# Kernel tuning notes

Hardware: AMD Instinct MI355X
Metric: run time of the kernel (lower is better)

The kernel has to match this reference:

```python
import jax, jax.numpy as jnp
import numpy as np

N = 50000      # nodes
E = 800000     # edges (before self-loops)
F_IN = 128     # input features
H = 4          # heads
C = 32         # hidden_dim per head
HC = H * C     # 128, concat width
G = 64         # graphs in batch
OUT = 10       # classes
NEG_SLOPE = 0.2  # PyG GATConv default negative_slope


def setup_inputs() -> dict:
    key = jax.random.key(0)
    ks = jax.random.split(key, 16)
    x = jax.random.normal(ks[0], (N, F_IN), dtype=jnp.float32)
    edge_index = jax.random.randint(ks[1], (2, E), 0, N, dtype=jnp.int32)
    batch = jnp.sort(jax.random.randint(ks[2], (N,), 0, G, dtype=jnp.int32))
    s = 0.05
    Ws = [
        jax.random.normal(ks[3], (F_IN, HC), jnp.float32) * s,
        jax.random.normal(ks[4], (HC, HC), jnp.float32) * s,
        jax.random.normal(ks[5], (HC, HC), jnp.float32) * s,
    ]
    a_srcs = [jax.random.normal(ks[6 + i], (H, C), jnp.float32) * s for i in range(3)]
    a_dsts = [jax.random.normal(ks[9 + i], (H, C), jnp.float32) * s for i in range(3)]
    biases = [jnp.zeros((HC,), jnp.float32) for _ in range(3)]
    Wh = jax.random.normal(ks[12], (HC, OUT), jnp.float32) * s
    bh = jnp.zeros((OUT,), jnp.float32)
    return {"x": x, "Ws": Ws, "a_srcs": a_srcs, "a_dsts": a_dsts,
            "biases": biases, "Wh": Wh, "bh": bh,
            "edge_index": edge_index, "batch": batch}


def gat_layer(x, W, a_src, a_dst, b, src, dst, n):
    # x: [N, F]; W: [F, H*C]; a_src/a_dst: [H, C]
    h = (x @ W).reshape(n, H, C)                     # [N, H, C]
    alpha_s = jnp.sum(h * a_src, axis=-1)            # [N, H]
    alpha_d = jnp.sum(h * a_dst, axis=-1)            # [N, H]
    e = jax.nn.leaky_relu(alpha_s[src] + alpha_d[dst], NEG_SLOPE)  # [E', H]
    # segment softmax over incoming edges (grouped by dst)
    emax = jax.ops.segment_max(e, dst, num_segments=n)             # [N, H]
    ex = jnp.exp(e - emax[dst])
    denom = jax.ops.segment_sum(ex, dst, num_segments=n)
    alpha = ex / denom[dst]                                        # [E', H]
    msg = h[src] * alpha[:, :, None]                               # [E', H, C]
    out = jax.ops.segment_sum(msg, dst, num_segments=n)            # [N, H, C]
    return out.reshape(n, HC) + b


def reference(x, Ws, a_srcs, a_dsts, biases, Wh, bh, edge_index, batch):
    n = x.shape[0]
    # PyG GATConv adds self-loops by default
    loops = jnp.arange(n, dtype=edge_index.dtype)
    src = jnp.concatenate([edge_index[0], loops])
    dst = jnp.concatenate([edge_index[1], loops])
    for i in range(3):
        x = jax.nn.relu(gat_layer(x, Ws[i], a_srcs[i], a_dsts[i], biases[i], src, dst, n))
        # dropout is identity in eval mode
    pooled = jax.ops.segment_sum(x, batch, num_segments=G)  # global_add_pool -> [G, HC]
    logits = pooled @ Wh + bh                                # [G, OUT]
    return logits
```

## Files before the change

### kernel.cpp

```cpp
#include <hip/hip_runtime.h>
#include <hip/hip_bf16.h>

#define HC 128
#define NHEAD 4
#define NEG 0.2f
#define CHUNK 4096

typedef unsigned int uint32;
typedef __attribute__((ext_vector_type(8))) short short8v;
typedef __attribute__((ext_vector_type(4))) float f32x4;

__device__ __forceinline__ float leaky(float v) { return v > 0.f ? v : NEG * v; }
__device__ __forceinline__ int clampi(int v, int lo, int hi) { return v < lo ? lo : (v > hi ? hi : v); }

__device__ __forceinline__ uint32 pack_bf16(float lo, float hi) {
  uint32 a = __float_as_uint(lo);
  uint32 b = __float_as_uint(hi);
  a = (a + 0x7FFFu + ((a >> 16) & 1u)) >> 16;
  b = (b + 0x7FFFu + ((b >> 16) & 1u)) & 0xFFFF0000u;
  return a | b;
}
__device__ __forceinline__ unsigned short bf16_1(float v) {
  uint32 a = __float_as_uint(v);
  return (unsigned short)((a + 0x7FFFu + ((a >> 16) & 1u)) >> 16);
}
__device__ __forceinline__ float2 unpack_bf16(uint32 u) {
  return make_float2(__uint_as_float(u << 16), __uint_as_float(u & 0xFFFF0000u));
}
__device__ __forceinline__ short8v as_s8(uint4 u) {
  union { uint4 a; short8v b; } c; c.a = u; return c.b;
}

#define WT_STRIDE 18432

__global__ __launch_bounds__(256) void zero_kernel(int* __restrict__ p, int n) {
  int i = blockIdx.x * 256 + threadIdx.x;
  int stride = gridDim.x * 256;
  for (; i < n; i += stride) p[i] = 0;
}

__global__ __launch_bounds__(256) void bincnt_lds(const int* __restrict__ dst, int* __restrict__ bcnt, int E, int n) {
  __shared__ int h[256];
  int t = threadIdx.x;
  h[t] = 0;
  __syncthreads();
  int e0 = blockIdx.x * CHUNK;
  int e1 = e0 + CHUNK < E ? e0 + CHUNK : E;
  for (int i = e0 + t; i < e1; i += 256) {
    int d = clampi(dst[i], 0, n - 1);
    atomicAdd(&h[d >> 8], 1);
  }
  __syncthreads();
  if (h[t] > 0) atomicAdd(&bcnt[t], h[t]);
}

__global__ __launch_bounds__(256) void bscan_kernel(const int* __restrict__ bcnt, int* __restrict__ bbase,
                                                    int* __restrict__ bcur, int NBKT) {
  __shared__ int part[256];
  int t = threadIdx.x;
  int c = (t < NBKT) ? bcnt[t] : 0;
  part[t] = c;
  __syncthreads();
  for (int off = 1; off < 256; off <<= 1) {
    int v = (t >= off) ? part[t - off] : 0;
    __syncthreads();
    part[t] += v;
    __syncthreads();
  }
  int excl = part[t] - c;
  if (t < NBKT) {
    bbase[t] = excl;
    bcur[t] = excl;
  }
}

__global__ __launch_bounds__(256) void binscatter_staged(const int* __restrict__ src, const int* __restrict__ dst,
                                                         int* __restrict__ bcur, int2* __restrict__ ebuf, int E, int n) {
  __shared__ int lcnt[256];
  __shared__ int lbase[256];
  int t = threadIdx.x;
  lcnt[t] = 0;
  __syncthreads();
  int e0 = blockIdx.x * CHUNK;
  int e1 = e0 + CHUNK < E ? e0 + CHUNK : E;
  for (int i = e0 + t; i < e1; i += 256) {
    int d = clampi(dst[i], 0, n - 1);
    atomicAdd(&lcnt[d >> 8], 1);
  }
  __syncthreads();
  int myc = lcnt[t];
  lbase[t] = (myc > 0) ? atomicAdd(&bcur[t], myc) : 0;
  __syncthreads();
  lcnt[t] = 0;
  __syncthreads();
  for (int i = e0 + t; i < e1; i += 256) {
    int d = clampi(dst[i], 0, n - 1);
    int s = clampi(src[i], 0, n - 1);
    int b = d >> 8;
    int pos = atomicAdd(&lcnt[b], 1);
    int p = lbase[b] + pos;
    if (p >= 0 && p < E) ebuf[p] = make_int2(s, d);
  }
}

__global__ __launch_bounds__(256) void bucket_finalize(const int2* __restrict__ ebuf, const int* __restrict__ bbase,
                                                       int* __restrict__ row_start, int* __restrict__ csr,
                                                       int NBKT, int E, int n) {
  __shared__ int cnt[256];
  __shared__ int part[256];
  __shared__ int cur[256];
  int b = blockIdx.x;
  int t = threadIdx.x;
  int start = bbase[b];
  int end = (b == NBKT - 1) ? E : bbase[b + 1];
  int d0 = b << 8;
  int ndst = n - d0; if (ndst > 256) ndst = 256;
  cnt[t] = 0;
  __syncthreads();
  for (int i = start + t; i < end; i += 256) {
    int d = ebuf[i].y - d0;
    if (d >= 0 && d < 256) atomicAdd(&cnt[d], 1);
  }
  __syncthreads();
  int c = cnt[t];
  part[t] = c;
  __syncthreads();
  for (int off = 1; off < 256; off <<= 1) {
    int v = (t >= off) ? part[t - off] : 0;
    __syncthreads();
    part[t] += v;
    __syncthreads();
  }
  int excl = part[t] - c;
  if (t < ndst) row_start[d0 + t] = start + excl;
  if (b == NBKT - 1 && t == 0) row_start[n] = E;
  cur[t] = start + excl;
  __syncthreads();
  for (int i = start + t; i < end; i += 256) {
    int2 pr = ebuf[i];
    int d = pr.y - d0;
    if (d >= 0 && d < 256) {
      int p = atomicAdd(&cur[d], 1);
      if (p >= 0 && p < E) csr[p] = pr.x;
    }
  }
}

__global__ __launch_bounds__(256) void hist_kernel(const int* __restrict__ dst, int* __restrict__ cnt, int E, int n) {
  int e = blockIdx.x * 256 + threadIdx.x;
  if (e < E) atomicAdd(&cnt[clampi(dst[e], 0, n - 1)], 1);
}
__global__ __launch_bounds__(256) void scan_pass1(const int* __restrict__ cnt, int* __restrict__ blocksum, int n) {
  __shared__ int red[256];
  int t = threadIdx.x;
  int i = blockIdx.x * 256 + t;
  red[t] = i < n ? cnt[i] : 0;
  __syncthreads();
  for (int off = 128; off >= 1; off >>= 1) {
    if (t < off) red[t] += red[t + off];
    __syncthreads();
  }
  if (t == 0) blocksum[blockIdx.x] = red[0];
}
__global__ __launch_bounds__(256) void scan_pass2(const int* __restrict__ blocksum, int* __restrict__ blockpre,
                                                  int* __restrict__ row_start, int NB, int n) {
  __shared__ int part[256];
  int t = threadIdx.x;
  int chunk = (NB + 255) >> 8;
  int lo = t * chunk; if (lo > NB) lo = NB;
  int hi = lo + chunk; if (hi > NB) hi = NB;
  int s = 0;
  for (int i = lo; i < hi; ++i) s += blocksum[i];
  part[t] = s;
  __syncthreads();
  for (int off = 1; off < 256; off <<= 1) {
    int v = (t >= off) ? part[t - off] : 0;
    __syncthreads();
    part[t] += v;
    __syncthreads();
  }
  int run = part[t] - s;
  for (int i = lo; i < hi; ++i) {
    blockpre[i] = run;
    run += blocksum[i];
  }
  if (t == 255) row_start[n] = part[255];
}
__global__ __launch_bounds__(256) void scan_pass3(const int* __restrict__ cnt, const int* __restrict__ blockpre,
                                                  int* __restrict__ row_start, int* __restrict__ cursor, int n) {
  __shared__ int part[256];
  int t = threadIdx.x;
  int i = blockIdx.x * 256 + t;
  int c = i < n ? cnt[i] : 0;
  part[t] = c;
  __syncthreads();
  for (int off = 1; off < 256; off <<= 1) {
    int v = (t >= off) ? part[t - off] : 0;
    __syncthreads();
    part[t] += v;
    __syncthreads();
  }
  int excl = part[t] - c;
  if (i < n) {
    int b = blockpre[blockIdx.x] + excl;
    row_start[i] = b;
    cursor[i] = b;
  }
}
__global__ __launch_bounds__(256) void scatter_kernel(const int* __restrict__ src, const int* __restrict__ dst,
                                                      int* __restrict__ cursor, int* __restrict__ csr, int E, int n) {
  int e = blockIdx.x * 256 + threadIdx.x;
  if (e < E) {
    int d = clampi(dst[e], 0, n - 1);
    int s = clampi(src[e], 0, n - 1);
    int p = atomicAdd(&cursor[d], 1);
    if (p >= 0 && p < E) csr[p] = s;
  }
}

__global__ __launch_bounds__(256) void prep_kernel(const float* __restrict__ x, const float* __restrict__ W0,
                                                   const float* __restrict__ W1, const float* __restrict__ W2,
                                                   const float* __restrict__ as0, const float* __restrict__ as1,
                                                   const float* __restrict__ as2, const float* __restrict__ ad0,
                                                   const float* __restrict__ ad1, const float* __restrict__ ad2,
                                                   uint32* __restrict__ X16, unsigned short* __restrict__ wt,
                                                   int* __restrict__ bcnt, float* __restrict__ pooled,
                                                   long long n64, int NC, int Gp) {
  long long id = (long long)blockIdx.x * 256 + threadIdx.x;
  if (id < n64) {
    float2 v = *(const float2*)&x[id * 2];
    X16[id] = pack_bf16(v.x, v.y);
    return;
  }
  long long id2l = id - n64;
  if (id2l < 3 * 16384) {
    int id2 = (int)id2l;
    int l = id2 >> 14;
    int r = id2 & 16383;
    int k = r >> 7, nc = r & 127;
    const float* W = l == 0 ? W0 : (l == 1 ? W1 : W2);
    wt[(size_t)l * WT_STRIDE + nc * 128 + k] = bf16_1(W[r]);
    return;
  }
  id2l -= 3 * 16384;
  if (id2l < 3 * 2048) {
    int id2 = (int)id2l;
    int l = id2 >> 11;
    int r = id2 & 2047;
    int col8 = r >> 7, k = r & 127;
    const float* W = l == 0 ? W0 : (l == 1 ? W1 : W2);
    unsigned short outv = 0;
    if (col8 < 8) {
      int h = col8 & 3;
      const float* av = (col8 < 4) ? (l == 0 ? as0 : (l == 1 ? as1 : as2))
                                   : (l == 0 ? ad0 : (l == 1 ? ad1 : ad2));
      float s = 0.f;
      for (int c = 0; c < 32; ++c) s += W[k * 128 + 32 * h + c] * av[32 * h + c];
      outv = bf16_1(s);
    }
    wt[(size_t)l * WT_STRIDE + (128 + col8) * 128 + k] = outv;
    return;
  }
  id2l -= 3 * 2048;
  if (id2l < NC) {
    bcnt[id2l] = 0;
    return;
  }
  id2l -= NC;
  if (id2l < (long long)Gp * 128) pooled[id2l] = 0.f;
}

__global__ __launch_bounds__(256) void gemm_mfma(const uint32* __restrict__ X16, const unsigned short* __restrict__ Wt,
                                                 uint32* __restrict__ H16, float* __restrict__ As,
                                                 float* __restrict__ Ad, int n) {
  int t = threadIdx.x;
  int wave = t >> 6, lane = t & 63;
  int l15 = lane & 15, lg = lane >> 4;
  int row0 = blockIdx.x * 64 + wave * 16;
  int arow = row0 + l15;
  if (arow >= n) arow = n - 1;
  const uint4* xr = (const uint4*)(X16 + (size_t)arow * 64);
  uint4 a[4];
#pragma unroll
  for (int kc = 0; kc < 4; ++kc) a[kc] = xr[kc * 4 + lg];
  f32x4 acc[9];
#pragma unroll
  for (int nb = 0; nb < 9; ++nb) acc[nb] = (f32x4){0.f, 0.f, 0.f, 0.f};
#pragma unroll
  for (int kc = 0; kc < 4; ++kc) {
    uint4 b[9];
#pragma unroll
    for (int nb = 0; nb < 9; ++nb) {
      int ncol = nb * 16 + l15;
      b[nb] = *(const uint4*)(Wt + (size_t)ncol * 128 + kc * 32 + lg * 8);
    }
#pragma unroll
    for (int nb = 0; nb < 9; ++nb)
      acc[nb] = __builtin_amdgcn_mfma_f32_16x16x32_bf16(as_s8(a[kc]), as_s8(b[nb]), acc[nb], 0, 0, 0);
  }
#pragma unroll
  for (int r = 0; r < 4; ++r) {
    int gr = row0 + lg * 4 + r;
    bool ok = gr < n;
#pragma unroll
    for (int nb = 0; nb < 8; ++nb) {
      float mine = acc[nb][r];
      float other = __shfl_xor(mine, 1);
      if (ok && (lane & 1) == 0) H16[(size_t)gr * 64 + nb * 8 + (l15 >> 1)] = pack_bf16(mine, other);
    }
    float av = acc[8][r];
    if (ok && l15 < 4) As[gr * 4 + l15] = av;
    if (ok && l15 >= 4 && l15 < 8) Ad[gr * 4 + (l15 - 4)] = av;
  }
}

template <bool OUTFP32>
__global__ __launch_bounds__(256) void agg_kernel(const uint32* __restrict__ H16, const float* __restrict__ As,
                                                  const float* __restrict__ Ad, const int* __restrict__ row_start,
                                                  const int* __restrict__ csr, const float* __restrict__ bias,
                                                  void* __restrict__ outv, int n) {
  int wid = (blockIdx.x * 256 + threadIdx.x) >> 6;
  int lane = threadIdx.x & 63;
  if (wid >= n) return;
  int base = row_start[wid];
  int deg = row_start[wid + 1] - base;
  if (deg < 0) deg = 0;
  int hsel = lane >> 4;
  float adsel = Ad[wid * 4 + hsel];
  float pself = __expf(leaky(As[wid * 4 + hsel] + adsel));
  float2 hv = unpack_bf16(H16[(size_t)wid * 64 + lane]);
  float den = pself;
  float acc0 = pself * hv.x, acc1 = pself * hv.y;
  for (int chunk = 0; chunk < deg; chunk += 64) {
    int j = chunk + lane;
    int smine = (j < deg) ? clampi(csr[base + j], 0, n - 1) : 0;
    int cnt_ = deg - chunk; if (cnt_ > 64) cnt_ = 64;
    float pm[4];
#pragma unroll
    for (int k = 0; k < 4; ++k) {
      pm[k] = 0.f;
      if (k * 16 < cnt_) {
        int slot = k * 16 + (lane & 15);
        int sk = __shfl(smine, slot);
        float e = As[sk * 4 + hsel];
        pm[k] = (slot < cnt_) ? __expf(leaky(e + adsel)) : 0.f;
      }
    }
#pragma unroll
    for (int k = 0; k < 4; ++k) {
      if (k * 16 >= cnt_) break;
#pragma unroll
      for (int b = 0; b < 2; ++b) {
        int u0 = k * 16 + b * 8;
        if (u0 >= cnt_) break;
        int ss[8];
        float aw[8];
        float2 h2[8];
#pragma unroll
        for (int i = 0; i < 8; ++i) {
          int u = u0 + i;
          int sv = __shfl(smine, u);
          float av = __shfl(pm[k], (lane & 48) + (u & 15));
          ss[i] = (u < cnt_) ? sv : 0;
          aw[i] = (u < cnt_) ? av : 0.f;
        }
#pragma unroll
        for (int i = 0; i < 8; ++i) h2[i] = unpack_bf16(H16[(size_t)((uint32)ss[i] * 64 + lane)]);
#pragma unroll
        for (int i = 0; i < 8; ++i) {
          den += aw[i];
          acc0 += aw[i] * h2[i].x;
          acc1 += aw[i] * h2[i].y;
        }
      }
    }
  }
  float inv = 1.f / den;
  float2 bv = *(const float2*)&bias[2 * lane];
  float r0v = fmaxf(acc0 * inv + bv.x, 0.f);
  float r1v = fmaxf(acc1 * inv + bv.y, 0.f);
  if constexpr (OUTFP32) {
    ((float2*)outv)[(size_t)wid * 64 + lane] = make_float2(r0v, r1v);
  } else {
    ((uint32*)outv)[(size_t)wid * 64 + lane] = pack_bf16(r0v, r1v);
  }
}

__global__ __launch_bounds__(128) void pool_kernel(const float* __restrict__ X, const int* __restrict__ batch,
                                                   float* __restrict__ pooled, int n, int G) {
  int c = threadIdx.x;
  int n0 = blockIdx.x * 64;
  if (n0 >= n) return;
  int end = n0 + 64 < n ? n0 + 64 : n;
  int curg = clampi(batch[n0], 0, G - 1);
  float acc = 0.f;
  for (int i = n0; i < end; ++i) {
    int g = clampi(batch[i], 0, G - 1);
    if (g != curg) {
      atomicAdd(&pooled[curg * 128 + c], acc);
      acc = 0.f;
      curg = g;
    }
    acc += X[(size_t)i * 128 + c];
  }
  atomicAdd(&pooled[curg * 128 + c], acc);
}

__global__ __launch_bounds__(64) void logits_kernel(const float* __restrict__ pooled, const float* __restrict__ Wh,
                                                    const float* __restrict__ bh, float* __restrict__ out) {
  int g = blockIdx.x, lane = threadIdx.x;
  float p0 = pooled[g * 128 + lane];
  float p1 = pooled[g * 128 + lane + 64];
  for (int o = 0; o < 10; ++o) {
    float v = p0 * Wh[lane * 10 + o] + p1 * Wh[(lane + 64) * 10 + o];
#pragma unroll
    for (int off = 32; off >= 1; off >>= 1) v += __shfl_xor(v, off);
    if (lane == 0) out[g * 10 + o] = v + bh[o];
  }
}

extern "C" void kernel_launch(void* const* d_in, const int* in_sizes, int n_in,
                              void* d_out, int out_size, void* d_ws, size_t ws_size,
                              hipStream_t stream) {
  const float *x, *Wl[3], *asr[3], *adr[3], *bias[3], *Wh, *bh;
  const int *edge_index, *batch;
  long long E_ll;
  if (n_in >= 17) {
    x = (const float*)d_in[0];
    for (int l = 0; l < 3; ++l) {
      Wl[l] = (const float*)d_in[1 + l];
      asr[l] = (const float*)d_in[4 + l];
      adr[l] = (const float*)d_in[7 + l];
      bias[l] = (const float*)d_in[10 + l];
    }
    Wh = (const float*)d_in[13];
    bh = (const float*)d_in[14];
    edge_index = (const int*)d_in[15];
    batch = (const int*)d_in[16];
    E_ll = (long long)in_sizes[15] / 2;
  } else if (n_in >= 9) {
    x = (const float*)d_in[0];
    const float* Wc = (const float*)d_in[1];
    const float* ac = (const float*)d_in[2];
    const float* dc = (const float*)d_in[3];
    const float* bc = (const float*)d_in[4];
    for (int l = 0; l < 3; ++l) {
      Wl[l] = Wc + (size_t)l * HC * HC;
      asr[l] = ac + (size_t)l * HC;
      adr[l] = dc + (size_t)l * HC;
      bias[l] = bc + (size_t)l * HC;
    }
    Wh = (const float*)d_in[5];
    bh = (const float*)d_in[6];
    edge_index = (const int*)d_in[7];
    batch = (const int*)d_in[8];
    E_ll = (long long)in_sizes[7] / 2;
  } else {
    zero_kernel<<<(out_size + 255) / 256, 256, 0, stream>>>((int*)d_out, out_size);
    return;
  }
  int N = in_sizes[0] / HC;
  int G = out_size / 10;
  if (N <= 0 || G <= 0 || E_ll <= 0 || E_ll > (1LL << 30)) {
    zero_kernel<<<(out_size + 255) / 256, 256, 0, stream>>>((int*)d_out, out_size);
    return;
  }
  int E = (int)E_ll;
  int NBKT = (N + 255) >> 8;
  int NB = (N + 255) / 256;
  bool staged = (NBKT <= 256);

  char* w = (char*)d_ws;
  size_t off = 0;
  auto take = [&](size_t bytes) -> char* {
    char* p = w + off;
    off = (off + bytes + 511) & ~(size_t)511;
    return p;
  };
  uint32* H16 = (uint32*)take((size_t)N * 64 * 4);
  uint32* X16 = (uint32*)take((size_t)N * 64 * 4);
  float* bufQ = (float*)take((size_t)N * HC * 4);
  uint32* Xa = (uint32*)bufQ;
  float* As = (float*)take((size_t)N * NHEAD * 4);
  float* Ad = (float*)take((size_t)N * NHEAD * 4);
  int* row_start = (int*)take((size_t)(N + 1) * 4);
  int* csr = (int*)take((size_t)E * 4);
  int2* ebuf = (int2*)take((size_t)E * 8);
  int* bcnt = (int*)take(256 * 4);
  int* bbase = (int*)take(256 * 4);
  int* bcur = (int*)take(256 * 4);
  int* cnt = (int*)take((size_t)N * 4);
  int* cursor = (int*)take((size_t)N * 4);
  int* blocksum = (int*)take((size_t)NB * 4);
  int* blockpre = (int*)take((size_t)NB * 4);
  float* pooled = (float*)take((size_t)G * HC * 4);
  unsigned short* wt16 = (unsigned short*)take((size_t)3 * WT_STRIDE * 2);

  if (off > ws_size) {
    zero_kernel<<<(out_size + 255) / 256, 256, 0, stream>>>((int*)d_out, out_size);
    return;
  }

  const int* esrc = edge_index;
  const int* edst = edge_index + E;

  long long n64 = (long long)N * 64;
  long long prep_items = n64 + 3 * 16384 + 3 * 2048 + 256 + (long long)G * 128;
  prep_kernel<<<(int)((prep_items + 255) / 256), 256, 0, stream>>>(
      x, Wl[0], Wl[1], Wl[2], asr[0], asr[1], asr[2], adr[0], adr[1], adr[2], Xa, wt16, bcnt, pooled, n64, 256, G);

  int echunks = (E + CHUNK - 1) / CHUNK;
  if (staged) {
    bincnt_lds<<<echunks, 256, 0, stream>>>(edst, bcnt, E, N);
    bscan_kernel<<<1, 256, 0, stream>>>(bcnt, bbase, bcur, NBKT);
    binscatter_staged<<<echunks, 256, 0, stream>>>(esrc, edst, bcur, ebuf, E, N);
    bucket_finalize<<<NBKT, 256, 0, stream>>>(ebuf, bbase, row_start, csr, NBKT, E, N);
  } else {
    zero_kernel<<<(N + 255) / 256, 256, 0, stream>>>(cnt, N);
    hist_kernel<<<(E + 255) / 256, 256, 0, stream>>>(edst, cnt, E, N);
    scan_pass1<<<NB, 256, 0, stream>>>(cnt, blocksum, N);
    scan_pass2<<<1, 256, 0, stream>>>(blocksum, blockpre, row_start, NB, N);
    scan_pass3<<<NB, 256, 0, stream>>>(cnt, blockpre, row_start, cursor, N);
    scatter_kernel<<<(E + 255) / 256, 256, 0, stream>>>(esrc, edst, cursor, csr, E, N);
  }

  int gemm_grid = (N + 63) / 64;
  int agg_grid = (N + 3) / 4;

  gemm_mfma<<<gemm_grid, 256, 0, stream>>>(Xa, wt16, H16, As, Ad, N);
  agg_kernel<false><<<agg_grid, 256, 0, stream>>>(H16, As, Ad, row_start, csr, bias[0], X16, N);
  gemm_mfma<<<gemm_grid, 256, 0, stream>>>(X16, wt16 + WT_STRIDE, H16, As, Ad, N);
  agg_kernel<false><<<agg_grid, 256, 0, stream>>>(H16, As, Ad, row_start, csr, bias[1], X16, N);
  gemm_mfma<<<gemm_grid, 256, 0, stream>>>(X16, wt16 + 2 * WT_STRIDE, H16, As, Ad, N);
  agg_kernel<true><<<agg_grid, 256, 0, stream>>>(H16, As, Ad, row_start, csr, bias[2], bufQ, N);

  pool_kernel<<<(N + 63) / 64, 128, 0, stream>>>(bufQ, batch, pooled, N, G);
  logits_kernel<<<G, 64, 0, stream>>>(pooled, Wh, bh, (float*)d_out);
}
```

Baseline: 277.9 us.

## Split GEMM column tiles across waves, fuse pooling with logits, trim agg bounds checks

The GEMM kernel now gives each pair of waves one 16-row tile and splits its 9 output column blocks 5/4 between them. This halves rows per block, doubles the grid and lowers per-wave register pressure. Pooling and the head projection are fused: each block reduces its per-graph partial sums through LDS, multiplies by Wh and atomically adds into the output, which prep_kernel pre-initialises with the bias. This removes the pooled buffer and the separate logits launch. The aggregation kernel drops the source-index clamp and per-slot validity selects, relying on zero-padded shuffled weights, which risks out-of-range reads if the CSR holds bad indices.

```diff
diff --git a/kernel.cpp b/kernel.cpp
--- a/kernel.cpp
+++ b/kernel.cpp
@@ -223,9 +223,9 @@
                                                    const float* __restrict__ as0, const float* __restrict__ as1,
                                                    const float* __restrict__ as2, const float* __restrict__ ad0,
                                                    const float* __restrict__ ad1, const float* __restrict__ ad2,
-                                                   uint32* __restrict__ X16, unsigned short* __restrict__ wt,
-                                                   int* __restrict__ bcnt, float* __restrict__ pooled,
-                                                   long long n64, int NC, int Gp) {
+                                                   const float* __restrict__ bh, uint32* __restrict__ X16,
+                                                   unsigned short* __restrict__ wt, int* __restrict__ bcnt,
+                                                   float* __restrict__ outp, long long n64, int NC, int Gp) {
   long long id = (long long)blockIdx.x * 256 + threadIdx.x;
   if (id < n64) {
     float2 v = *(const float2*)&x[id * 2];
@@ -267,7 +267,7 @@
     return;
   }
   id2l -= NC;
-  if (id2l < (long long)Gp * 128) pooled[id2l] = 0.f;
+  if (id2l < (long long)Gp * 10) outp[id2l] = bh[id2l % 10];
 }
 
 __global__ __launch_bounds__(256) void gemm_mfma(const uint32* __restrict__ X16, const unsigned short* __restrict__ Wt,
@@ -276,41 +276,48 @@
   int t = threadIdx.x;
   int wave = t >> 6, lane = t & 63;
   int l15 = lane & 15, lg = lane >> 4;
-  int row0 = blockIdx.x * 64 + wave * 16;
+  int grp = wave >> 1, half = wave & 1;
+  int row0 = blockIdx.x * 32 + grp * 16;
   int arow = row0 + l15;
   if (arow >= n) arow = n - 1;
   const uint4* xr = (const uint4*)(X16 + (size_t)arow * 64);
   uint4 a[4];
 #pragma unroll
   for (int kc = 0; kc < 4; ++kc) a[kc] = xr[kc * 4 + lg];
-  f32x4 acc[9];
-#pragma unroll
-  for (int nb = 0; nb < 9; ++nb) acc[nb] = (f32x4){0.f, 0.f, 0.f, 0.f};
+  const int NT = half ? 4 : 5;
+  f32x4 acc[5];
+#pragma unroll
+  for (int ti = 0; ti < 5; ++ti) acc[ti] = (f32x4){0.f, 0.f, 0.f, 0.f};
 #pragma unroll
   for (int kc = 0; kc < 4; ++kc) {
-    uint4 b[9];
-#pragma unroll
-    for (int nb = 0; nb < 9; ++nb) {
-      int ncol = nb * 16 + l15;
-      b[nb] = *(const uint4*)(Wt + (size_t)ncol * 128 + kc * 32 + lg * 8);
-    }
-#pragma unroll
-    for (int nb = 0; nb < 9; ++nb)
-      acc[nb] = __builtin_amdgcn_mfma_f32_16x16x32_bf16(as_s8(a[kc]), as_s8(b[nb]), acc[nb], 0, 0, 0);
+    uint4 b[5];
+#pragma unroll
+    for (int ti = 0; ti < 5; ++ti) {
+      if (ti < NT) {
+        int basecol = half ? (4 + ti) * 16 : (ti < 4 ? ti * 16 : 128);
+        b[ti] = *(const uint4*)(Wt + (size_t)(basecol + l15) * 128 + kc * 32 + lg * 8);
+      }
+    }
+#pragma unroll
+    for (int ti = 0; ti < 5; ++ti)
+      if (ti < NT) acc[ti] = __builtin_amdgcn_mfma_f32_16x16x32_bf16(as_s8(a[kc]), as_s8(b[ti]), acc[ti], 0, 0, 0);
   }
 #pragma unroll
   for (int r = 0; r < 4; ++r) {
     int gr = row0 + lg * 4 + r;
     bool ok = gr < n;
 #pragma unroll
-    for (int nb = 0; nb < 8; ++nb) {
-      float mine = acc[nb][r];
+    for (int ti = 0; ti < 4; ++ti) {
+      int nb = half * 4 + ti;
+      float mine = acc[ti][r];
       float other = __shfl_xor(mine, 1);
       if (ok && (lane & 1) == 0) H16[(size_t)gr * 64 + nb * 8 + (l15 >> 1)] = pack_bf16(mine, other);
     }
-    float av = acc[8][r];
-    if (ok && l15 < 4) As[gr * 4 + l15] = av;
-    if (ok && l15 >= 4 && l15 < 8) Ad[gr * 4 + (l15 - 4)] = av;
+    if (half == 0) {
+      float av = acc[4][r];
+      if (ok && l15 < 4) As[gr * 4 + l15] = av;
+      if (ok && l15 >= 4 && l15 < 8) Ad[gr * 4 + (l15 - 4)] = av;
+    }
   }
 }
 
@@ -333,7 +340,7 @@
   float acc0 = pself * hv.x, acc1 = pself * hv.y;
   for (int chunk = 0; chunk < deg; chunk += 64) {
     int j = chunk + lane;
-    int smine = (j < deg) ? clampi(csr[base + j], 0, n - 1) : 0;
+    int smine = (j < deg) ? csr[base + j] : 0;
     int cnt_ = deg - chunk; if (cnt_ > 64) cnt_ = 64;
     float pm[4];
 #pragma unroll
@@ -358,11 +365,8 @@
         float2 h2[8];
 #pragma unroll
         for (int i = 0; i < 8; ++i) {
-          int u = u0 + i;
-          int sv = __shfl(smine, u);
-          float av = __shfl(pm[k], (lane & 48) + (u & 15));
-          ss[i] = (u < cnt_) ? sv : 0;
-          aw[i] = (u < cnt_) ? av : 0.f;
+          ss[i] = __shfl(smine, u0 + i);
+          aw[i] = __shfl(pm[k], (lane & 48) + (b * 8 + i));
         }
 #pragma unroll
         for (int i = 0; i < 8; ++i) h2[i] = unpack_bf16(H16[(size_t)((uint32)ss[i] * 64 + lane)]);
@@ -386,36 +390,32 @@
   }
 }
 
-__global__ __launch_bounds__(128) void pool_kernel(const float* __restrict__ X, const int* __restrict__ batch,
-                                                   float* __restrict__ pooled, int n, int G) {
+__global__ __launch_bounds__(128) void pool_logits(const float* __restrict__ X, const int* __restrict__ batch,
+                                                   const float* __restrict__ Wh, float* __restrict__ out,
+                                                   int n, int G) {
+  __shared__ float red[128];
   int c = threadIdx.x;
   int n0 = blockIdx.x * 64;
   if (n0 >= n) return;
   int end = n0 + 64 < n ? n0 + 64 : n;
   int curg = clampi(batch[n0], 0, G - 1);
   float acc = 0.f;
-  for (int i = n0; i < end; ++i) {
-    int g = clampi(batch[i], 0, G - 1);
+  for (int i = n0; i <= end; ++i) {
+    int g = (i < end) ? clampi(batch[i], 0, G - 1) : -1;
     if (g != curg) {
-      atomicAdd(&pooled[curg * 128 + c], acc);
+      red[c] = acc;
+      __syncthreads();
+      if (c < 10) {
+        float s = 0.f;
+#pragma unroll 16
+        for (int cc = 0; cc < 128; ++cc) s += red[cc] * Wh[cc * 10 + c];
+        atomicAdd(&out[curg * 10 + c], s);
+      }
+      __syncthreads();
       acc = 0.f;
       curg = g;
     }
-    acc += X[(size_t)i * 128 + c];
-  }
-  atomicAdd(&pooled[curg * 128 + c], acc);
-}
-
-__global__ __launch_bounds__(64) void logits_kernel(const float* __restrict__ pooled, const float* __restrict__ Wh,
-                                                    const float* __restrict__ bh, float* __restrict__ out) {
-  int g = blockIdx.x, lane = threadIdx.x;
-  float p0 = pooled[g * 128 + lane];
-  float p1 = pooled[g * 128 + lane + 64];
-  for (int o = 0; o < 10; ++o) {
-    float v = p0 * Wh[lane * 10 + o] + p1 * Wh[(lane + 64) * 10 + o];
-#pragma unroll
-    for (int off = 32; off >= 1; off >>= 1) v += __shfl_xor(v, off);
-    if (lane == 0) out[g * 10 + o] = v + bh[o];
+    if (i < end) acc += X[(size_t)i * 128 + c];
   }
 }
 
@@ -493,7 +493,6 @@
   int* cursor = (int*)take((size_t)N * 4);
   int* blocksum = (int*)take((size_t)NB * 4);
   int* blockpre = (int*)take((size_t)NB * 4);
-  float* pooled = (float*)take((size_t)G * HC * 4);
   unsigned short* wt16 = (unsigned short*)take((size_t)3 * WT_STRIDE * 2);
 
   if (off > ws_size) {
@@ -505,9 +504,10 @@
   const int* edst = edge_index + E;
 
   long long n64 = (long long)N * 64;
-  long long prep_items = n64 + 3 * 16384 + 3 * 2048 + 256 + (long long)G * 128;
+  long long prep_items = n64 + 3 * 16384 + 3 * 2048 + 256 + (long long)G * 10;
   prep_kernel<<<(int)((prep_items + 255) / 256), 256, 0, stream>>>(
-      x, Wl[0], Wl[1], Wl[2], asr[0], asr[1], asr[2], adr[0], adr[1], adr[2], Xa, wt16, bcnt, pooled, n64, 256, G);
+      x, Wl[0], Wl[1], Wl[2], asr[0], asr[1], asr[2], adr[0], adr[1], adr[2], bh,
+      Xa, wt16, bcnt, (float*)d_out, n64, 256, G);
 
   int echunks = (E + CHUNK - 1) / CHUNK;
   if (staged) {
@@ -524,7 +524,7 @@
     scatter_kernel<<<(E + 255) / 256, 256, 0, stream>>>(esrc, edst, cursor, csr, E, N);
   }
 
-  int gemm_grid = (N + 63) / 64;
+  int gemm_grid = (N + 31) / 32;
   int agg_grid = (N + 3) / 4;
 
   gemm_mfma<<<gemm_grid, 256, 0, stream>>>(Xa, wt16, H16, As, Ad, N);
@@ -534,6 +534,5 @@
   gemm_mfma<<<gemm_grid, 256, 0, stream>>>(X16, wt16 + 2 * WT_STRIDE, H16, As, Ad, N);
   agg_kernel<true><<<agg_grid, 256, 0, stream>>>(H16, As, Ad, row_start, csr, bias[2], bufQ, N);
 
-  pool_kernel<<<(N + 63) / 64, 128, 0, stream>>>(bufQ, batch, pooled, N, G);
-  logits_kernel<<<G, 64, 0, stream>>>(pooled, Wh, bh, (float*)d_out);
-}
+  pool_logits<<<(N + 63) / 64, 128, 0, stream>>>(bufQ, batch, Wh, (float*)d_out, N, G);
+}
```

New measurement: 261.5 us. 5.9% less time.

## Split GEMM columns across waves, widen agg gather batches, fuse pooling into last layer

Applied to the files above, without the earlier changes.

The GEMM now has each block handle 16 rows, with its four waves splitting the output column tiles, so each wave holds fewer accumulators and the grid grows fourfold. The aggregation loop issues 16 neighbor row gathers per batch instead of 8 and drops the clamp on neighbor indices. The final layer atomically adds its results straight into per-graph pooled sums, removing the fp32 intermediate buffer and the separate pool kernel. In exchange it adds many contended atomics on only 64 graph rows, and unclamped CSR indices could read out of bounds.

```diff
diff --git a/kernel.cpp b/kernel.cpp
--- a/kernel.cpp
+++ b/kernel.cpp
@@ -276,49 +276,56 @@
   int t = threadIdx.x;
   int wave = t >> 6, lane = t & 63;
   int l15 = lane & 15, lg = lane >> 4;
-  int row0 = blockIdx.x * 64 + wave * 16;
+  int row0 = blockIdx.x * 16;
   int arow = row0 + l15;
   if (arow >= n) arow = n - 1;
   const uint4* xr = (const uint4*)(X16 + (size_t)arow * 64);
   uint4 a[4];
 #pragma unroll
   for (int kc = 0; kc < 4; ++kc) a[kc] = xr[kc * 4 + lg];
-  f32x4 acc[9];
-#pragma unroll
-  for (int nb = 0; nb < 9; ++nb) acc[nb] = (f32x4){0.f, 0.f, 0.f, 0.f};
+  const int NT = (wave == 0) ? 3 : 2;
+  f32x4 acc[3];
+#pragma unroll
+  for (int ti = 0; ti < 3; ++ti) acc[ti] = (f32x4){0.f, 0.f, 0.f, 0.f};
 #pragma unroll
   for (int kc = 0; kc < 4; ++kc) {
-    uint4 b[9];
-#pragma unroll
-    for (int nb = 0; nb < 9; ++nb) {
-      int ncol = nb * 16 + l15;
-      b[nb] = *(const uint4*)(Wt + (size_t)ncol * 128 + kc * 32 + lg * 8);
-    }
-#pragma unroll
-    for (int nb = 0; nb < 9; ++nb)
-      acc[nb] = __builtin_amdgcn_mfma_f32_16x16x32_bf16(as_s8(a[kc]), as_s8(b[nb]), acc[nb], 0, 0, 0);
+    uint4 b[3];
+#pragma unroll
+    for (int ti = 0; ti < 3; ++ti) {
+      if (ti < NT) {
+        int basecol = (ti < 2) ? (2 * wave + ti) * 16 : 128;
+        b[ti] = *(const uint4*)(Wt + (size_t)(basecol + l15) * 128 + kc * 32 + lg * 8);
+      }
+    }
+#pragma unroll
+    for (int ti = 0; ti < 3; ++ti)
+      if (ti < NT) acc[ti] = __builtin_amdgcn_mfma_f32_16x16x32_bf16(as_s8(a[kc]), as_s8(b[ti]), acc[ti], 0, 0, 0);
   }
 #pragma unroll
   for (int r = 0; r < 4; ++r) {
     int gr = row0 + lg * 4 + r;
     bool ok = gr < n;
 #pragma unroll
-    for (int nb = 0; nb < 8; ++nb) {
-      float mine = acc[nb][r];
+    for (int ti = 0; ti < 2; ++ti) {
+      int nb = 2 * wave + ti;
+      float mine = acc[ti][r];
       float other = __shfl_xor(mine, 1);
       if (ok && (lane & 1) == 0) H16[(size_t)gr * 64 + nb * 8 + (l15 >> 1)] = pack_bf16(mine, other);
     }
-    float av = acc[8][r];
-    if (ok && l15 < 4) As[gr * 4 + l15] = av;
-    if (ok && l15 >= 4 && l15 < 8) Ad[gr * 4 + (l15 - 4)] = av;
-  }
-}
-
-template <bool OUTFP32>
+    if (wave == 0) {
+      float av = acc[2][r];
+      if (ok && l15 < 4) As[gr * 4 + l15] = av;
+      if (ok && l15 >= 4 && l15 < 8) Ad[gr * 4 + (l15 - 4)] = av;
+    }
+  }
+}
+
+template <bool POOL>
 __global__ __launch_bounds__(256) void agg_kernel(const uint32* __restrict__ H16, const float* __restrict__ As,
                                                   const float* __restrict__ Ad, const int* __restrict__ row_start,
                                                   const int* __restrict__ csr, const float* __restrict__ bias,
-                                                  void* __restrict__ outv, int n) {
+                                                  const int* __restrict__ batch, void* __restrict__ outv,
+                                                  int n, int G) {
   int wid = (blockIdx.x * 256 + threadIdx.x) >> 6;
   int lane = threadIdx.x & 63;
   if (wid >= n) return;
@@ -333,45 +340,31 @@
   float acc0 = pself * hv.x, acc1 = pself * hv.y;
   for (int chunk = 0; chunk < deg; chunk += 64) {
     int j = chunk + lane;
-    int smine = (j < deg) ? clampi(csr[base + j], 0, n - 1) : 0;
+    int smine = (j < deg) ? csr[base + j] : 0;
     int cnt_ = deg - chunk; if (cnt_ > 64) cnt_ = 64;
-    float pm[4];
 #pragma unroll
     for (int k = 0; k < 4; ++k) {
-      pm[k] = 0.f;
-      if (k * 16 < cnt_) {
+      if (k * 16 >= cnt_) break;
+      float pmk;
+      {
         int slot = k * 16 + (lane & 15);
         int sk = __shfl(smine, slot);
         float e = As[sk * 4 + hsel];
-        pm[k] = (slot < cnt_) ? __expf(leaky(e + adsel)) : 0.f;
+        pmk = (slot < cnt_) ? __expf(leaky(e + adsel)) : 0.f;
       }
-    }
-#pragma unroll
-    for (int k = 0; k < 4; ++k) {
-      if (k * 16 >= cnt_) break;
-#pragma unroll
-      for (int b = 0; b < 2; ++b) {
-        int u0 = k * 16 + b * 8;
-        if (u0 >= cnt_) break;
-        int ss[8];
-        float aw[8];
-        float2 h2[8];
-#pragma unroll
-        for (int i = 0; i < 8; ++i) {
-          int u = u0 + i;
-          int sv = __shfl(smine, u);
-          float av = __shfl(pm[k], (lane & 48) + (u & 15));
-          ss[i] = (u < cnt_) ? sv : 0;
-          aw[i] = (u < cnt_) ? av : 0.f;
-        }
-#pragma unroll
-        for (int i = 0; i < 8; ++i) h2[i] = unpack_bf16(H16[(size_t)((uint32)ss[i] * 64 + lane)]);
-#pragma unroll
-        for (int i = 0; i < 8; ++i) {
-          den += aw[i];
-          acc0 += aw[i] * h2[i].x;
-          acc1 += aw[i] * h2[i].y;
-        }
+      int ss[16];
+      uint32 h2[16];
+#pragma unroll
+      for (int i = 0; i < 16; ++i) ss[i] = __shfl(smine, k * 16 + i);
+#pragma unroll
+      for (int i = 0; i < 16; ++i) h2[i] = H16[(size_t)((uint32)ss[i] * 64 + lane)];
+#pragma unroll
+      for (int i = 0; i < 16; ++i) {
+        float aw = __shfl(pmk, (lane & 48) + i);
+        float2 hh = unpack_bf16(h2[i]);
+        den += aw;
+        acc0 += aw * hh.x;
+        acc1 += aw * hh.y;
       }
     }
   }
@@ -379,31 +372,14 @@
   float2 bv = *(const float2*)&bias[2 * lane];
   float r0v = fmaxf(acc0 * inv + bv.x, 0.f);
   float r1v = fmaxf(acc1 * inv + bv.y, 0.f);
-  if constexpr (OUTFP32) {
-    ((float2*)outv)[(size_t)wid * 64 + lane] = make_float2(r0v, r1v);
+  if constexpr (POOL) {
+    int g = clampi(batch[wid], 0, G - 1);
+    float* pooled = (float*)outv;
+    atomicAdd(&pooled[g * 128 + 2 * lane], r0v);
+    atomicAdd(&pooled[g * 128 + 2 * lane + 1], r1v);
   } else {
     ((uint32*)outv)[(size_t)wid * 64 + lane] = pack_bf16(r0v, r1v);
   }
-}
-
-__global__ __launch_bounds__(128) void pool_kernel(const float* __restrict__ X, const int* __restrict__ batch,
-                                                   float* __restrict__ pooled, int n, int G) {
-  int c = threadIdx.x;
-  int n0 = blockIdx.x * 64;
-  if (n0 >= n) return;
-  int end = n0 + 64 < n ? n0 + 64 : n;
-  int curg = clampi(batch[n0], 0, G - 1);
-  float acc = 0.f;
-  for (int i = n0; i < end; ++i) {
-    int g = clampi(batch[i], 0, G - 1);
-    if (g != curg) {
-      atomicAdd(&pooled[curg * 128 + c], acc);
-      acc = 0.f;
-      curg = g;
-    }
-    acc += X[(size_t)i * 128 + c];
-  }
-  atomicAdd(&pooled[curg * 128 + c], acc);
 }
 
 __global__ __launch_bounds__(64) void logits_kernel(const float* __restrict__ pooled, const float* __restrict__ Wh,
@@ -479,8 +455,7 @@
   };
   uint32* H16 = (uint32*)take((size_t)N * 64 * 4);
   uint32* X16 = (uint32*)take((size_t)N * 64 * 4);
-  float* bufQ = (float*)take((size_t)N * HC * 4);
-  uint32* Xa = (uint32*)bufQ;
+  uint32* Xa = (uint32*)take((size_t)N * 64 * 4);
   float* As = (float*)take((size_t)N * NHEAD * 4);
   float* Ad = (float*)take((size_t)N * NHEAD * 4);
   int* row_start = (int*)take((size_t)(N + 1) * 4);
@@ -507,7 +482,8 @@
   long long n64 = (long long)N * 64;
   long long prep_items = n64 + 3 * 16384 + 3 * 2048 + 256 + (long long)G * 128;
   prep_kernel<<<(int)((prep_items + 255) / 256), 256, 0, stream>>>(
-      x, Wl[0], Wl[1], Wl[2], asr[0], asr[1], asr[2], adr[0], adr[1], adr[2], Xa, wt16, bcnt, pooled, n64, 256, G);
+      x, Wl[0], Wl[1], Wl[2], asr[0], asr[1], asr[2], adr[0], adr[1], adr[2],
+      Xa, wt16, bcnt, pooled, n64, 256, G);
 
   int echunks = (E + CHUNK - 1) / CHUNK;
   if (staged) {
@@ -524,16 +500,15 @@
     scatter_kernel<<<(E + 255) / 256, 256, 0, stream>>>(esrc, edst, cursor, csr, E, N);
   }
 
-  int gemm_grid = (N + 63) / 64;
+  int gemm_grid = (N + 15) / 16;
   int agg_grid = (N + 3) / 4;
 
   gemm_mfma<<<gemm_grid, 256, 0, stream>>>(Xa, wt16, H16, As, Ad, N);
-  agg_kernel<false><<<agg_grid, 256, 0, stream>>>(H16, As, Ad, row_start, csr, bias[0], X16, N);
+  agg_kernel<false><<<agg_grid, 256, 0, stream>>>(H16, As, Ad, row_start, csr, bias[0], batch, X16, N, G);
   gemm_mfma<<<gemm_grid, 256, 0, stream>>>(X16, wt16 + WT_STRIDE, H16, As, Ad, N);
-  agg_kernel<false><<<agg_grid, 256, 0, stream>>>(H16, As, Ad, row_start, csr, bias[1], X16, N);
+  agg_kernel<false><<<agg_grid, 256, 0, stream>>>(H16, As, Ad, row_start, csr, bias[1], batch, X16, N, G);
   gemm_mfma<<<gemm_grid, 256, 0, stream>>>(X16, wt16 + 2 * WT_STRIDE, H16, As, Ad, N);
-  agg_kernel<true><<<agg_grid, 256, 0, stream>>>(H16, As, Ad, row_start, csr, bias[2], bufQ, N);
-
-  pool_kernel<<<(N + 63) / 64, 128, 0, stream>>>(bufQ, batch, pooled, N, G);
+  agg_kernel<true><<<agg_grid, 256, 0, stream>>>(H16, As, Ad, row_start, csr, bias[2], batch, pooled, N, G);
+
   logits_kernel<<<G, 64, 0, stream>>>(pooled, Wh, bh, (float*)d_out);
 }
```

Result: slower. 340.5 us (+22.5%).
